# Performance work log

Measured on AMD Instinct MI355X. Metric: run time of the kernel, lower is better.

## Reference

```python
import jax, jax.numpy as jnp
import numpy as np

B, LQ, LIM = 4, 640, 1296
D_MODEL, NHEAD, DFF, MAX_DIST = 768, 12, 3072, 100
DK = D_MODEL // NHEAD
EPS = 1e-5


def _layer_norm(x, g, b):
    mu = jnp.mean(x, axis=-1, keepdims=True)
    var = jnp.mean(jnp.square(x - mu), axis=-1, keepdims=True)
    return (x - mu) * jax.lax.rsqrt(var + EPS) * g + b


def setup_inputs() -> dict:
    key = jax.random.key(0)
    ks = jax.random.split(key, 24)
    s = 0.02
    inp = {
        "docqa": jax.random.normal(ks[0], (B, LQ, D_MODEL), jnp.float32),
        "im_tokens": jax.random.normal(ks[1], (B, LIM, D_MODEL), jnp.float32),
        "docqa_x": jax.random.randint(ks[2], (B, LQ), 0, 1000, jnp.int32),
        "docqa_y": jax.random.randint(ks[3], (B, LQ), 0, 1000, jnp.int32),
        "im_tokens_x": jax.random.randint(ks[4], (B, LIM), 0, 1000, jnp.int32),
        "im_tokens_y": jax.random.randint(ks[5], (B, LIM), 0, 1000, jnp.int32),
        # attention projection params
        "Wq": jax.random.normal(ks[6], (D_MODEL, D_MODEL), jnp.float32) * s,
        "bq": jnp.zeros((D_MODEL,), jnp.float32),
        "Wk": jax.random.normal(ks[7], (D_MODEL, D_MODEL), jnp.float32) * s,
        "bk": jnp.zeros((D_MODEL,), jnp.float32),
        "Wv": jax.random.normal(ks[8], (D_MODEL, D_MODEL), jnp.float32) * s,
        "bv": jnp.zeros((D_MODEL,), jnp.float32),
        "Wo": jax.random.normal(ks[9], (D_MODEL, D_MODEL), jnp.float32) * s,
        "bo": jnp.zeros((D_MODEL,), jnp.float32),
        # relative position bias tables: (2*max_dist+1, nhead) per axis
        "bias_x": jax.random.normal(ks[10], (2 * MAX_DIST + 1, NHEAD), jnp.float32) * s,
        "bias_y": jax.random.normal(ks[11], (2 * MAX_DIST + 1, NHEAD), jnp.float32) * s,
        # FFN
        "W1": jax.random.normal(ks[12], (D_MODEL, DFF), jnp.float32) * s,
        "b1": jnp.zeros((DFF,), jnp.float32),
        "W2": jax.random.normal(ks[13], (DFF, D_MODEL), jnp.float32) * s,
        "b2": jnp.zeros((D_MODEL,), jnp.float32),
        # LayerNorms
        "g1": jnp.ones((D_MODEL,), jnp.float32),
        "be1": jnp.zeros((D_MODEL,), jnp.float32),
        "g2": jnp.ones((D_MODEL,), jnp.float32),
        "be2": jnp.zeros((D_MODEL,), jnp.float32),
    }
    return inp


def reference(docqa, im_tokens, docqa_x, docqa_y, im_tokens_x, im_tokens_y,
              Wq, bq, Wk, bk, Wv, bv, Wo, bo, bias_x, bias_y,
              W1, b1, W2, b2, g1, be1, g2, be2):
    # keys/values attend over concatenated image tokens + docqa tokens
    full = jnp.concatenate([im_tokens, docqa], axis=1)            # (B, Lk, D)
    full_x = jnp.concatenate([im_tokens_x, docqa_x], axis=1)      # (B, Lk)
    full_y = jnp.concatenate([im_tokens_y, docqa_y], axis=1)

    q = (docqa @ Wq + bq).reshape(B, LQ, NHEAD, DK)               # (B,Lq,H,Dk)
    k = (full @ Wk + bk).reshape(B, LQ + LIM, NHEAD, DK)
    v = (full @ Wv + bv).reshape(B, LQ + LIM, NHEAD, DK)

    scores = jnp.einsum("bqhd,bkhd->bhqk", q, k) / jnp.sqrt(jnp.float32(DK))

    # relative-position bias, clamped to [-max_dist, max_dist]
    rel_x = jnp.clip(docqa_x[:, :, None] - full_x[:, None, :], -MAX_DIST, MAX_DIST) + MAX_DIST
    rel_y = jnp.clip(docqa_y[:, :, None] - full_y[:, None, :], -MAX_DIST, MAX_DIST) + MAX_DIST
    pos_bias = bias_x[rel_x] + bias_y[rel_y]                      # (B,Lq,Lk,H)
    scores = scores + jnp.transpose(pos_bias, (0, 3, 1, 2))       # (B,H,Lq,Lk)

    attn = jax.nn.softmax(scores, axis=-1)
    ctx = jnp.einsum("bhqk,bkhd->bqhd", attn, v).reshape(B, LQ, D_MODEL)
    attn_out = ctx @ Wo + bo

    # residual + norm + FFN + residual + norm (dropout=0 in eval)
    src = _layer_norm(docqa + attn_out, g1, be1)
    ffn = jnp.maximum(src @ W1 + b1, 0.0) @ W2 + b2
    src = _layer_norm(src + ffn, g2, be2)
    return src
```

## Files before the change

kernel.cpp:

```cpp
#include <hip/hip_runtime.h>
#include <hip/hip_bf16.h>

constexpr int B      = 4;
constexpr int LQ     = 640;
constexpr int LIM    = 1296;
constexpr int LK     = LQ + LIM;
constexpr int DM     = 768;
constexpr int NHEAD  = 12;
constexpr int DK     = 64;
constexpr int DFF    = 3072;
constexpr int MAXD   = 100;
constexpr int M_DOC  = B * LQ;
constexpr int M_FULL = B * LK;
constexpr size_t ML_CNT = (size_t)B * NHEAD * LQ;

typedef __attribute__((ext_vector_type(8))) short bf16x8_t;
typedef __attribute__((ext_vector_type(4))) float f32x4_t;

__device__ __forceinline__ float b2f(__hip_bfloat16 x) { return __bfloat162float(x); }

__device__ __forceinline__ float ldf(const void* p, size_t i, int f32flag) {
    return f32flag ? ((const float*)p)[i]
                   : b2f(((const __hip_bfloat16*)p)[i]);
}

__device__ __forceinline__ void gl_lds16(const void* g, void* l) {
    __builtin_amdgcn_global_load_lds(
        (const __attribute__((address_space(1))) unsigned int*)g,
        (__attribute__((address_space(3))) unsigned int*)l, 16, 0, 0);
}

__global__ __launch_bounds__(256)
void prep_kernel(const void* __restrict__ g1, int* __restrict__ flagp,
                 const int* __restrict__ dqx, const int* __restrict__ dqy,
                 const int* __restrict__ imx, const int* __restrict__ imy,
                 int* __restrict__ cx, int* __restrict__ cy)
{
    if (blockIdx.x == 0 && threadIdx.x == 0) {
        unsigned u = *(const unsigned*)g1;
        *flagp = ((u & 0xFFFFu) == 0u) ? 1 : 0;
    }
    int idx = blockIdx.x * 256 + threadIdx.x;
    for (; idx < B * LK; idx += gridDim.x * 256) {
        int b = idx / LK, l = idx - b * LK;
        cx[idx] = (l < LIM) ? imx[b * LIM + l] : dqx[b * LQ + l - LIM];
        cy[idx] = (l < LIM) ? imy[b * LIM + l] : dqy[b * LQ + l - LIM];
    }
}

__device__ __forceinline__ void wtrans_tile(const void* W, __hip_bfloat16* Wt,
                                            int f32, int K, int N, int n0, int k0,
                                            __hip_bfloat16 (*t)[33])
{
    const int tx = threadIdx.x & 31, ty = threadIdx.x >> 5;
#pragma unroll
    for (int j = 0; j < 4; ++j) {
        int k = ty + j * 8;
        t[k][tx] = __float2bfloat16(ldf(W, (size_t)(k0 + k) * N + n0 + tx, f32));
    }
    __syncthreads();
#pragma unroll
    for (int j = 0; j < 4; ++j) {
        int n = ty + j * 8;
        Wt[(size_t)(n0 + n) * K + k0 + tx] = t[tx][n];
    }
}

__global__ __launch_bounds__(256)
void wtransA_kernel(const void* __restrict__ Wq, const void* __restrict__ Wk,
                    const void* __restrict__ Wv, const void* __restrict__ Wo,
                    __hip_bfloat16* __restrict__ Wt3, __hip_bfloat16* __restrict__ WtO,
                    const int* __restrict__ flagp)
{
    __shared__ __hip_bfloat16 t[32][33];
    const int f32 = *flagp;
    const int bx  = blockIdx.x;
    const int wid = bx / 576;
    const int tt  = bx % 576;
    const void* W = (wid == 0) ? Wq : (wid == 1) ? Wk : (wid == 2) ? Wv : Wo;
    __hip_bfloat16* dst = (wid == 3) ? WtO : Wt3 + (size_t)wid * DM * DM;
    wtrans_tile(W, dst, f32, DM, DM, (tt % 24) * 32, (tt / 24) * 32, t);
}

__global__ __launch_bounds__(256)
void wtransW_kernel(const void* __restrict__ W1, const void* __restrict__ W2,
                    __hip_bfloat16* __restrict__ W1t, __hip_bfloat16* __restrict__ W2t,
                    const int* __restrict__ flagp)
{
    __shared__ __hip_bfloat16 t[32][33];
    const int f32 = *flagp;
    int bx = blockIdx.x;
    const bool second = bx >= 2304;
    const void* W = second ? W2 : W1;
    __hip_bfloat16* dst = second ? W2t : W1t;
    const int K = second ? DFF : DM;
    const int N = second ? DM : DFF;
    const int tt = second ? bx - 2304 : bx;
    const int nt = N / 32;
    wtrans_tile(W, dst, f32, K, N, (tt % nt) * 32, (tt / nt) * 32, t);
}

__global__ __launch_bounds__(256)
void qkv_gemm(const void* __restrict__ Aim,
              const void* __restrict__ Adoc,
              const __hip_bfloat16* __restrict__ Wt3,
              const void* __restrict__ bq,
              const void* __restrict__ bk,
              const void* __restrict__ bv,
              __hip_bfloat16* __restrict__ qb,
              __hip_bfloat16* __restrict__ kb,
              __hip_bfloat16* __restrict__ vtb,
              const int* __restrict__ flagp)
{
    __shared__ __hip_bfloat16 Als[128 * 32];
    __shared__ __hip_bfloat16 Bls[128 * 32];

    const int f32  = *flagp;
    const int tid  = threadIdx.x;
    const int lane = tid & 63;
    const int wave = tid >> 6;
    const int quad = lane >> 4;
    const int c16  = lane & 15;
    const int n0   = blockIdx.x * 128;
    const int m0   = blockIdx.y * 128;
    const int wm   = (wave >> 1) * 64;
    const int wn   = (wave & 1) * 64;
    constexpr int K = DM;

    f32x4_t acc[4][4] = {};

    for (int k0 = 0; k0 < K; k0 += 32) {
#pragma unroll
        for (int p = 0; p < 2; ++p) {
            const int lin = p * 64 + lane;
            int row = wave * 32 + (lin >> 2);
            int gr  = m0 + row; if (gr > M_FULL - 1) gr = M_FULL - 1;
            const int kcol = k0 + (lin & 3) * 8;
            int bb = gr / LK;
            int l  = gr - bb * LK;
            const void* base; size_t roff;
            if (l < LIM) { base = Aim;  roff = (size_t)(bb * LIM + l) * K; }
            else         { base = Adoc; roff = (size_t)(bb * LQ + (l - LIM)) * K; }
            union { bf16x8_t v; __hip_bfloat16 h[8]; } pk;
            if (f32) {
                const float4* fp = (const float4*)((const float*)base + roff + kcol);
                float4 a = fp[0], b4 = fp[1];
                pk.h[0] = __float2bfloat16(a.x);  pk.h[1] = __float2bfloat16(a.y);
                pk.h[2] = __float2bfloat16(a.z);  pk.h[3] = __float2bfloat16(a.w);
                pk.h[4] = __float2bfloat16(b4.x); pk.h[5] = __float2bfloat16(b4.y);
                pk.h[6] = __float2bfloat16(b4.z); pk.h[7] = __float2bfloat16(b4.w);
            } else {
                pk.v = *(const bf16x8_t*)((const __hip_bfloat16*)base + roff + kcol);
            }
            *(bf16x8_t*)(Als + wave * 1024 + (size_t)lin * 8) = pk.v;
        }
#pragma unroll
        for (int p = 0; p < 2; ++p) {
            const int lin = p * 64 + lane;
            const int row = wave * 32 + (lin >> 2);
            gl_lds16(Wt3 + (size_t)(n0 + row) * K + k0 + (lin & 3) * 8,
                     Bls + wave * 1024 + p * 512);
        }
        __syncthreads();

        bf16x8_t af[4], bfr[4];
#pragma unroll
        for (int i = 0; i < 4; ++i)
            af[i] = *(const bf16x8_t*)(Als + (wm + i * 16 + c16) * 32 + quad * 8);
#pragma unroll
        for (int j = 0; j < 4; ++j)
            bfr[j] = *(const bf16x8_t*)(Bls + (wn + j * 16 + c16) * 32 + quad * 8);
#pragma unroll
        for (int i = 0; i < 4; ++i)
#pragma unroll
            for (int j = 0; j < 4; ++j)
                acc[i][j] = __builtin_amdgcn_mfma_f32_16x16x32_bf16(af[i], bfr[j], acc[i][j], 0, 0, 0);
        __syncthreads();
    }

    const int seg = n0 / DM;
    const void* bptr = (seg == 0) ? bq : (seg == 1) ? bk : bv;
#pragma unroll
    for (int j = 0; j < 4; ++j) {
        const int col  = n0 + wn + j * 16 + c16;
        const int ncol = col - seg * DM;
        const float bj = ldf(bptr, ncol, f32);
        if (seg == 2) {
            const int h = ncol >> 6, d = ncol & 63;
#pragma unroll
            for (int i = 0; i < 4; ++i) {
                const int rowb = m0 + wm + i * 16 + quad * 4;
                const int bb0  = rowb / LK;
                const int l0   = rowb - bb0 * LK;
                if (l0 + 3 < LK && rowb + 3 < M_FULL) {
                    union { ushort4 u4; __hip_bfloat16 hh[4]; } pk;
#pragma unroll
                    for (int r = 0; r < 4; ++r)
                        pk.hh[r] = __float2bfloat16(acc[i][j][r] + bj);
                    *(ushort4*)(vtb + ((size_t)((bb0 * NHEAD + h) * DK + d)) * LK + l0) = pk.u4;
                } else {
#pragma unroll
                    for (int r = 0; r < 4; ++r) {
                        const int row = rowb + r;
                        if (row < M_FULL) {
                            int bb = row / LK, l = row - bb * LK;
                            vtb[((size_t)((bb * NHEAD + h) * DK + d)) * LK + l] =
                                __float2bfloat16(acc[i][j][r] + bj);
                        }
                    }
                }
            }
        } else {
            const float scl = (seg == 0) ? 0.125f : 1.f;
#pragma unroll
            for (int i = 0; i < 4; ++i) {
                const int rowb = m0 + wm + i * 16 + quad * 4;
#pragma unroll
                for (int r = 0; r < 4; ++r) {
                    const int row = rowb + r;
                    if (row < M_FULL) {
                        __hip_bfloat16 hv = __float2bfloat16((acc[i][j][r] + bj) * scl);
                        if (seg == 1) kb[(size_t)row * DM + ncol] = hv;
                        else {
                            int bb = row / LK, l = row - bb * LK;
                            if (l >= LIM)
                                qb[(size_t)(bb * LQ + (l - LIM)) * DM + ncol] = hv;
                        }
                    }
                }
            }
        }
    }
}

__global__ __launch_bounds__(256)
void mfma_gemm_relu(const __hip_bfloat16* __restrict__ Abf,
                    const __hip_bfloat16* __restrict__ Wt,
                    const void* __restrict__ bias,
                    __hip_bfloat16* __restrict__ Cc,
                    const int* __restrict__ flagp,
                    int M, int N, int K)
{
    __shared__ __hip_bfloat16 Als[128 * 32];
    __shared__ __hip_bfloat16 Bls[128 * 32];

    const int f32  = *flagp;
    const int tid  = threadIdx.x;
    const int lane = tid & 63;
    const int wave = tid >> 6;
    const int quad = lane >> 4;
    const int c16  = lane & 15;
    const int n0   = blockIdx.x * 128;
    const int m0   = blockIdx.y * 128;
    const int wm   = (wave >> 1) * 64;
    const int wn   = (wave & 1) * 64;

    f32x4_t acc[4][4] = {};

    for (int k0 = 0; k0 < K; k0 += 32) {
#pragma unroll
        for (int p = 0; p < 2; ++p) {
            const int lin = p * 64 + lane;
            int row = wave * 32 + (lin >> 2);
            int gr  = m0 + row; if (gr > M - 1) gr = M - 1;
            gl_lds16(Abf + (size_t)gr * K + k0 + (lin & 3) * 8, Als + wave * 1024 + p * 512);
        }
#pragma unroll
        for (int p = 0; p < 2; ++p) {
            const int lin = p * 64 + lane;
            const int row = wave * 32 + (lin >> 2);
            gl_lds16(Wt + (size_t)(n0 + row) * K + k0 + (lin & 3) * 8,
                     Bls + wave * 1024 + p * 512);
        }
        __syncthreads();

        bf16x8_t af[4], bfr[4];
#pragma unroll
        for (int i = 0; i < 4; ++i)
            af[i] = *(const bf16x8_t*)(Als + (wm + i * 16 + c16) * 32 + quad * 8);
#pragma unroll
        for (int j = 0; j < 4; ++j)
            bfr[j] = *(const bf16x8_t*)(Bls + (wn + j * 16 + c16) * 32 + quad * 8);
#pragma unroll
        for (int i = 0; i < 4; ++i)
#pragma unroll
            for (int j = 0; j < 4; ++j)
                acc[i][j] = __builtin_amdgcn_mfma_f32_16x16x32_bf16(af[i], bfr[j], acc[i][j], 0, 0, 0);
        __syncthreads();
    }

#pragma unroll
    for (int j = 0; j < 4; ++j) {
        const int col = n0 + wn + j * 16 + c16;
        const float bj = ldf(bias, col, f32);
#pragma unroll
        for (int i = 0; i < 4; ++i) {
            const int rowb = m0 + wm + i * 16 + quad * 4;
#pragma unroll
            for (int r = 0; r < 4; ++r) {
                const int row = rowb + r;
                if (row < M) {
                    float v = fmaxf(acc[i][j][r] + bj, 0.f);
                    Cc[(size_t)row * N + col] = __float2bfloat16(v);
                }
            }
        }
    }
}

__global__ __launch_bounds__(256)
void sk_gemm(const __hip_bfloat16* __restrict__ Abf,
             const __hip_bfloat16* __restrict__ Wt,
             float* __restrict__ Cc,
             int M, int N, int K, int S)
{
    __shared__ __hip_bfloat16 Als[128 * 32];
    __shared__ __hip_bfloat16 Bls[128 * 32];

    const int tid  = threadIdx.x;
    const int lane = tid & 63;
    const int wave = tid >> 6;
    const int quad = lane >> 4;
    const int c16  = lane & 15;
    const int n0   = blockIdx.x * 128;
    const int m0   = blockIdx.y * 128;
    const int wm   = (wave >> 1) * 64;
    const int wn   = (wave & 1) * 64;
    const int kchunk = K / S;
    const int kbeg = blockIdx.z * kchunk;

    f32x4_t acc[4][4] = {};

    for (int k0 = kbeg; k0 < kbeg + kchunk; k0 += 32) {
#pragma unroll
        for (int p = 0; p < 2; ++p) {
            const int lin = p * 64 + lane;
            int row = wave * 32 + (lin >> 2);
            int gr  = m0 + row; if (gr > M - 1) gr = M - 1;
            gl_lds16(Abf + (size_t)gr * K + k0 + (lin & 3) * 8, Als + wave * 1024 + p * 512);
        }
#pragma unroll
        for (int p = 0; p < 2; ++p) {
            const int lin = p * 64 + lane;
            const int row = wave * 32 + (lin >> 2);
            gl_lds16(Wt + (size_t)(n0 + row) * K + k0 + (lin & 3) * 8,
                     Bls + wave * 1024 + p * 512);
        }
        __syncthreads();

        bf16x8_t af[4], bfr[4];
#pragma unroll
        for (int i = 0; i < 4; ++i)
            af[i] = *(const bf16x8_t*)(Als + (wm + i * 16 + c16) * 32 + quad * 8);
#pragma unroll
        for (int j = 0; j < 4; ++j)
            bfr[j] = *(const bf16x8_t*)(Bls + (wn + j * 16 + c16) * 32 + quad * 8);
#pragma unroll
        for (int i = 0; i < 4; ++i)
#pragma unroll
            for (int j = 0; j < 4; ++j)
                acc[i][j] = __builtin_amdgcn_mfma_f32_16x16x32_bf16(af[i], bfr[j], acc[i][j], 0, 0, 0);
        __syncthreads();
    }

#pragma unroll
    for (int j = 0; j < 4; ++j) {
        const int col = n0 + wn + j * 16 + c16;
#pragma unroll
        for (int i = 0; i < 4; ++i) {
            const int rowb = m0 + wm + i * 16 + quad * 4;
#pragma unroll
            for (int r = 0; r < 4; ++r) {
                const int row = rowb + r;
                if (row < M) atomicAdd(&Cc[(size_t)row * N + col], acc[i][j][r]);
            }
        }
    }
}

__global__ __launch_bounds__(256)
void attn_part_kernel(const __hip_bfloat16* __restrict__ Qb,
                      const __hip_bfloat16* __restrict__ Kb,
                      const __hip_bfloat16* __restrict__ Vtb,
                      const int* __restrict__ cx, const int* __restrict__ cy,
                      const void* __restrict__ bias_x,
                      const void* __restrict__ bias_y,
                      __hip_bfloat16* __restrict__ p0,
                      __hip_bfloat16* __restrict__ p1,
                      float* __restrict__ mlbase,
                      const int* __restrict__ flagp)
{
    constexpr int QT = 64, KT = 64;
    constexpr int QROW = 72;
    __shared__ __hip_bfloat16 Ps[QT * QROW];
    __shared__ float bxs[2 * MAXD + 1], bys[2 * MAXD + 1];

    const int f32  = *flagp;
    const int tid  = threadIdx.x;
    const int lane = tid & 63;
    const int wave = tid >> 6;
    const int quad = lane >> 4;
    const int c16  = lane & 15;
    const int h    = blockIdx.y;
    const int b    = blockIdx.z & 3;
    const int s    = blockIdx.z >> 2;
    const int q0   = blockIdx.x * QT;
    const int kbeg = s * 1024;
    const int kend = s ? LK : 1024;

    __hip_bfloat16* Op = s ? p1 : p0;
    float* mp = mlbase + (size_t)s * 2 * ML_CNT;
    float* lp = mp + ML_CNT;

    for (int i = tid; i < 2 * MAXD + 1; i += 256) {
        bxs[i] = ldf(bias_x, (size_t)i * NHEAD + h, f32);
        bys[i] = ldf(bias_y, (size_t)i * NHEAD + h, f32);
    }

    const __hip_bfloat16* qrow = Qb + ((size_t)(b * LQ + q0 + wave * 16 + c16)) * DM + h * DK;
    const bf16x8_t aq0 = *(const bf16x8_t*)(qrow + quad * 8);
    const bf16x8_t aq1 = *(const bf16x8_t*)(qrow + 32 + quad * 8);
    int qx[4], qy[4];
#pragma unroll
    for (int r = 0; r < 4; ++r) {
        const int qi = b * LK + LIM + q0 + wave * 16 + quad * 4 + r;
        qx[r] = cx[qi]; qy[r] = cy[qi];
    }
    const __hip_bfloat16* vrow = Vtb + ((size_t)((b * NHEAD + h) * DK)) * LK;

    __syncthreads();

    f32x4_t O[4] = {};
    float m_r[4], l_r[4];
#pragma unroll
    for (int r = 0; r < 4; ++r) { m_r[r] = -1e30f; l_r[r] = 0.f; }

    for (int k0 = kbeg; k0 < kend; k0 += KT) {
        f32x4_t S[4];
#pragma unroll
        for (int jn = 0; jn < 4; ++jn) {
            int krow = k0 + jn * 16 + c16; if (krow > LK - 1) krow = LK - 1;
            const __hip_bfloat16* kr = Kb + ((size_t)(b * LK + krow)) * DM + h * DK;
            bf16x8_t bk0 = *(const bf16x8_t*)(kr + quad * 8);
            bf16x8_t bk1 = *(const bf16x8_t*)(kr + 32 + quad * 8);
            f32x4_t acc = {0.f, 0.f, 0.f, 0.f};
            acc = __builtin_amdgcn_mfma_f32_16x16x32_bf16(aq0, bk0, acc, 0, 0, 0);
            acc = __builtin_amdgcn_mfma_f32_16x16x32_bf16(aq1, bk1, acc, 0, 0, 0);
            S[jn] = acc;
        }
#pragma unroll
        for (int jn = 0; jn < 4; ++jn) {
            const int kg = k0 + jn * 16 + c16;
            const bool ok = kg < LK;
            const int kgc = ok ? kg : LK - 1;
            const int kx = cx[b * LK + kgc], ky = cy[b * LK + kgc];
#pragma unroll
            for (int r = 0; r < 4; ++r) {
                int rx = min(max(qx[r] - kx, -MAXD), MAXD) + MAXD;
                int ry = min(max(qy[r] - ky, -MAXD), MAXD) + MAXD;
                float v = S[jn][r] + bxs[rx] + bys[ry];
                S[jn][r] = ok ? v : -1e30f;
            }
        }
        float alpha[4];
#pragma unroll
        for (int r = 0; r < 4; ++r) {
            float mx = fmaxf(fmaxf(S[0][r], S[1][r]), fmaxf(S[2][r], S[3][r]));
            mx = fmaxf(mx, __shfl_xor(mx, 1));
            mx = fmaxf(mx, __shfl_xor(mx, 2));
            mx = fmaxf(mx, __shfl_xor(mx, 4));
            mx = fmaxf(mx, __shfl_xor(mx, 8));
            const float mt = fmaxf(m_r[r], mx);
            const float al = __expf(m_r[r] - mt);
            float sum = 0.f;
#pragma unroll
            for (int jn = 0; jn < 4; ++jn) {
                float p = __expf(S[jn][r] - mt);
                S[jn][r] = p;
                sum += p;
            }
            sum += __shfl_xor(sum, 1);
            sum += __shfl_xor(sum, 2);
            sum += __shfl_xor(sum, 4);
            sum += __shfl_xor(sum, 8);
            m_r[r] = mt;
            l_r[r] = l_r[r] * al + sum;
            alpha[r] = al;
        }
#pragma unroll
        for (int jn = 0; jn < 4; ++jn)
#pragma unroll
            for (int r = 0; r < 4; ++r)
                Ps[(wave * 16 + quad * 4 + r) * QROW + jn * 16 + c16] = __float2bfloat16(S[jn][r]);
#pragma unroll
        for (int jd = 0; jd < 4; ++jd)
#pragma unroll
            for (int r = 0; r < 4; ++r) O[jd][r] *= alpha[r];
        bf16x8_t ap0 = *(const bf16x8_t*)(Ps + (wave * 16 + c16) * QROW + quad * 8);
        bf16x8_t ap1 = *(const bf16x8_t*)(Ps + (wave * 16 + c16) * QROW + 32 + quad * 8);
        int kc0 = k0 + quad * 8;      if (kc0 > LK - 8) kc0 = LK - 8;
        int kc1 = k0 + 32 + quad * 8; if (kc1 > LK - 8) kc1 = LK - 8;
#pragma unroll
        for (int jd = 0; jd < 4; ++jd) {
            const __hip_bfloat16* vr = vrow + (size_t)(jd * 16 + c16) * LK;
            bf16x8_t bv0 = *(const bf16x8_t*)(vr + kc0);
            bf16x8_t bv1 = *(const bf16x8_t*)(vr + kc1);
            O[jd] = __builtin_amdgcn_mfma_f32_16x16x32_bf16(ap0, bv0, O[jd], 0, 0, 0);
            O[jd] = __builtin_amdgcn_mfma_f32_16x16x32_bf16(ap1, bv1, O[jd], 0, 0, 0);
        }
    }

#pragma unroll
    for (int r = 0; r < 4; ++r) {
        const int ql = wave * 16 + quad * 4 + r;
        const size_t grow = (size_t)(b * LQ + q0 + ql);
#pragma unroll
        for (int jd = 0; jd < 4; ++jd)
            Op[grow * DM + h * DK + jd * 16 + c16] = __float2bfloat16(O[jd][r]);
        if (c16 == 0) {
            size_t mli = ((size_t)b * NHEAD + h) * LQ + q0 + ql;
            mp[mli] = m_r[r];
            lp[mli] = l_r[r];
        }
    }
}

__global__ __launch_bounds__(256)
void attn_merge_kernel(const __hip_bfloat16* __restrict__ p0,
                       const __hip_bfloat16* __restrict__ p1,
                       const float* __restrict__ mlbase,
                       __hip_bfloat16* __restrict__ ctx,
                       float* __restrict__ aof)
{
    const int row = blockIdx.x;
    const int b = row / LQ, q = row - b * LQ;
    const int tid = threadIdx.x;
#pragma unroll
    for (int i = 0; i < 3; ++i) {
        const int c = tid + i * 256;
        const int h = c >> 6;
        const size_t mli = ((size_t)b * NHEAD + h) * LQ + q;
        const float m0 = mlbase[mli],              l0 = mlbase[ML_CNT + mli];
        const float m1 = mlbase[2 * ML_CNT + mli], l1 = mlbase[3 * ML_CNT + mli];
        const float mm = fmaxf(m0, m1);
        const float w0 = __expf(m0 - mm), w1 = __expf(m1 - mm);
        const float denom = l0 * w0 + l1 * w1;
        const size_t idx = (size_t)row * DM + c;
        const float v = (b2f(p0[idx]) * w0 + b2f(p1[idx]) * w1) / denom;
        ctx[idx] = __float2bfloat16(v);
        aof[idx] = 0.f;
    }
}

template<int MODE>
__global__ __launch_bounds__(256)
void ln_kernel(const void* __restrict__ Xin,
               const __hip_bfloat16* __restrict__ Xb,
               const float* __restrict__ Xf2f,
               const void* __restrict__ bias2,
               const void* __restrict__ g,
               const void* __restrict__ be,
               __hip_bfloat16* __restrict__ outb,
               void* __restrict__ outv,
               float* __restrict__ zbuf,
               const int* __restrict__ flagp)
{
    __shared__ float red1[256], red2[256];
    const int f32 = *flagp;
    const int row = blockIdx.x;
    const int tid = threadIdx.x;

    float x[3];
#pragma unroll
    for (int i = 0; i < 3; ++i) {
        int c = tid + i * 256;
        size_t idx = (size_t)row * DM + c;
        float a  = (MODE == 0) ? ldf(Xin, idx, f32) : b2f(Xb[idx]);
        x[i] = a + Xf2f[idx] + ldf(bias2, c, f32);
    }
    float s1 = x[0] + x[1] + x[2];
    float s2 = x[0] * x[0] + x[1] * x[1] + x[2] * x[2];
    red1[tid] = s1;
    red2[tid] = s2;
    __syncthreads();
    for (int off = 128; off > 0; off >>= 1) {
        if (tid < off) {
            red1[tid] += red1[tid + off];
            red2[tid] += red2[tid + off];
        }
        __syncthreads();
    }
    float mu   = red1[0] * (1.f / DM);
    float var  = red2[0] * (1.f / DM) - mu * mu;
    float rstd = rsqrtf(var + 1e-5f);
#pragma unroll
    for (int i = 0; i < 3; ++i) {
        int c = tid + i * 256;
        size_t idx = (size_t)row * DM + c;
        float v = (x[i] - mu) * rstd * ldf(g, c, f32) + ldf(be, c, f32);
        if (MODE == 0) {
            outb[idx] = __float2bfloat16(v);
            zbuf[idx] = 0.f;
        } else {
            if (f32) ((float*)outv)[idx] = v;
            else     ((__hip_bfloat16*)outv)[idx] = __float2bfloat16(v);
        }
    }
}

extern "C" void kernel_launch(void* const* d_in, const int* in_sizes, int n_in,
                              void* d_out, int out_size, void* d_ws, size_t ws_size,
                              hipStream_t stream)
{
    const void* docqa = d_in[0];
    const void* im    = d_in[1];
    const int* dqx = (const int*)d_in[2];
    const int* dqy = (const int*)d_in[3];
    const int* imx = (const int*)d_in[4];
    const int* imy = (const int*)d_in[5];
    const void* Wq = d_in[6];
    const void* bq = d_in[7];
    const void* Wk = d_in[8];
    const void* bk = d_in[9];
    const void* Wv = d_in[10];
    const void* bv = d_in[11];
    const void* Wo = d_in[12];
    const void* bo = d_in[13];
    const void* bias_x = d_in[14];
    const void* bias_y = d_in[15];
    const void* W1 = d_in[16];
    const void* b1 = d_in[17];
    const void* W2 = d_in[18];
    const void* b2 = d_in[19];
    const void* g1  = d_in[20];
    const void* be1 = d_in[21];
    const void* g2  = d_in[22];
    const void* be2 = d_in[23];

    char* w = (char*)d_ws;
    int*            flagp = (int*)w;
    __hip_bfloat16* qb  = (__hip_bfloat16*)(w + 256);
    __hip_bfloat16* kb  = qb + (size_t)M_DOC  * DM;
    __hip_bfloat16* vtb = kb + (size_t)M_FULL * DM;
    __hip_bfloat16* cb  = vtb + (size_t)M_FULL * DM;
    char* cbB = (char*)cb;

    __hip_bfloat16* Wt3  = cb;
    __hip_bfloat16* p0   = cb;
    __hip_bfloat16* p1   = (__hip_bfloat16*)(cbB + 3932160);
    float*          mlb  = (float*)(cbB + 7864320);
    __hip_bfloat16* WtO  = (__hip_bfloat16*)(cbB + 8355840);
    int*            cxp  = (int*)(cbB + 9535488);
    int*            cyp  = cxp + (size_t)B * LK;
    __hip_bfloat16* ctx  = cb;
    __hip_bfloat16* src1 = cb;
    float*          fof  = (float*)(cbB + 3932160);
    float*          aof  = (float*)vtb;
    __hip_bfloat16* W1t  = vtb;
    __hip_bfloat16* W2t  = vtb + (size_t)DFF * DM;
    __hip_bfloat16* mid  = qb;

    dim3 blk(256);

    prep_kernel<<<dim3(32), blk, 0, stream>>>(g1, flagp, dqx, dqy, imx, imy, cxp, cyp);
    wtransA_kernel<<<dim3(4 * 576), blk, 0, stream>>>(Wq, Wk, Wv, Wo, Wt3, WtO, flagp);
    qkv_gemm<<<dim3(3 * DM / 128, (M_FULL + 127) / 128), blk, 0, stream>>>(
        im, docqa, Wt3, bq, bk, bv, qb, kb, vtb, flagp);
    attn_part_kernel<<<dim3(LQ / 64, NHEAD, B * 2), blk, 0, stream>>>(
        qb, kb, vtb, cxp, cyp, bias_x, bias_y, p0, p1, mlb, flagp);
    attn_merge_kernel<<<dim3(M_DOC), blk, 0, stream>>>(p0, p1, mlb, ctx, aof);
    sk_gemm<<<dim3(DM / 128, M_DOC / 128, 4), blk, 0, stream>>>(
        ctx, WtO, aof, M_DOC, DM, DM, 4);
    ln_kernel<0><<<dim3(M_DOC), blk, 0, stream>>>(
        docqa, nullptr, aof, bo, g1, be1, src1, nullptr, fof, flagp);
    wtransW_kernel<<<dim3(2 * 2304), blk, 0, stream>>>(W1, W2, W1t, W2t, flagp);
    mfma_gemm_relu<<<dim3(DFF / 128, M_DOC / 128), blk, 0, stream>>>(
        src1, W1t, b1, mid, flagp, M_DOC, DFF, DM);
    sk_gemm<<<dim3(DM / 128, M_DOC / 128, 4), blk, 0, stream>>>(
        mid, W2t, fof, M_DOC, DM, DFF, 4);
    ln_kernel<1><<<dim3(M_DOC), blk, 0, stream>>>(
        nullptr, src1, fof, b2, g2, be2, nullptr, d_out, nullptr, flagp);
}
```

Measured before the change: 451.2 us.

## Pre-convert concatenated input to bf16 and load QKV GEMM A via LDS DMA

```diff
diff --git a/kernel.cpp b/kernel.cpp
--- a/kernel.cpp
+++ b/kernel.cpp
@@ -31,21 +31,34 @@
 }
 
 __global__ __launch_bounds__(256)
-void prep_kernel(const void* __restrict__ g1, int* __restrict__ flagp,
-                 const int* __restrict__ dqx, const int* __restrict__ dqy,
-                 const int* __restrict__ imx, const int* __restrict__ imy,
-                 int* __restrict__ cx, int* __restrict__ cy)
-{
-    if (blockIdx.x == 0 && threadIdx.x == 0) {
-        unsigned u = *(const unsigned*)g1;
-        *flagp = ((u & 0xFFFFu) == 0u) ? 1 : 0;
-    }
-    int idx = blockIdx.x * 256 + threadIdx.x;
-    for (; idx < B * LK; idx += gridDim.x * 256) {
-        int b = idx / LK, l = idx - b * LK;
-        cx[idx] = (l < LIM) ? imx[b * LIM + l] : dqx[b * LQ + l - LIM];
-        cy[idx] = (l < LIM) ? imy[b * LIM + l] : dqy[b * LQ + l - LIM];
-    }
+void prep_conv_kernel(const void* __restrict__ g1, int* __restrict__ flagp,
+                      const void* __restrict__ im, const void* __restrict__ docqa,
+                      __hip_bfloat16* __restrict__ fullA)
+{
+    const bool f32 = ((*(const unsigned*)g1) & 0xFFFFu) == 0u;
+    if (blockIdx.x == 0 && threadIdx.x == 0) *flagp = f32 ? 1 : 0;
+
+    const int chunk = blockIdx.x * 256 + threadIdx.x;
+    if (chunk >= M_FULL * (DM / 8)) return;
+    const int row = chunk / (DM / 8);
+    const int col = (chunk - row * (DM / 8)) * 8;
+    const int b   = row / LK;
+    const int l   = row - b * LK;
+    const size_t srow = (l < LIM) ? ((size_t)(b * LIM + l)) * DM
+                                  : ((size_t)(b * LQ + (l - LIM))) * DM;
+    const void* src = (l < LIM) ? im : docqa;
+    union { bf16x8_t v; __hip_bfloat16 h[8]; } pk;
+    if (f32) {
+        const float4* fp = (const float4*)((const float*)src + srow + col);
+        float4 a = fp[0], c = fp[1];
+        pk.h[0] = __float2bfloat16(a.x); pk.h[1] = __float2bfloat16(a.y);
+        pk.h[2] = __float2bfloat16(a.z); pk.h[3] = __float2bfloat16(a.w);
+        pk.h[4] = __float2bfloat16(c.x); pk.h[5] = __float2bfloat16(c.y);
+        pk.h[6] = __float2bfloat16(c.z); pk.h[7] = __float2bfloat16(c.w);
+    } else {
+        pk.v = *(const bf16x8_t*)((const __hip_bfloat16*)src + srow + col);
+    }
+    *(bf16x8_t*)(fullA + (size_t)row * DM + col) = pk.v;
 }
 
 __device__ __forceinline__ void wtrans_tile(const void* W, __hip_bfloat16* Wt,
@@ -67,19 +80,27 @@
 }
 
 __global__ __launch_bounds__(256)
-void wtransA_kernel(const void* __restrict__ Wq, const void* __restrict__ Wk,
-                    const void* __restrict__ Wv, const void* __restrict__ Wo,
-                    __hip_bfloat16* __restrict__ Wt3, __hip_bfloat16* __restrict__ WtO,
+void wtrans3_kernel(const void* __restrict__ Wq, const void* __restrict__ Wk,
+                    const void* __restrict__ Wv, __hip_bfloat16* __restrict__ Wt3,
                     const int* __restrict__ flagp)
 {
     __shared__ __hip_bfloat16 t[32][33];
     const int f32 = *flagp;
-    const int bx  = blockIdx.x;
-    const int wid = bx / 576;
-    const int tt  = bx % 576;
-    const void* W = (wid == 0) ? Wq : (wid == 1) ? Wk : (wid == 2) ? Wv : Wo;
-    __hip_bfloat16* dst = (wid == 3) ? WtO : Wt3 + (size_t)wid * DM * DM;
-    wtrans_tile(W, dst, f32, DM, DM, (tt % 24) * 32, (tt / 24) * 32, t);
+    const int wid = blockIdx.x / 576;
+    const int tt  = blockIdx.x % 576;
+    const void* W = (wid == 0) ? Wq : (wid == 1) ? Wk : Wv;
+    wtrans_tile(W, Wt3 + (size_t)wid * DM * DM, f32, DM, DM,
+                (tt % 24) * 32, (tt / 24) * 32, t);
+}
+
+__global__ __launch_bounds__(256)
+void wtransO_kernel(const void* __restrict__ Wo, __hip_bfloat16* __restrict__ WtO,
+                    const int* __restrict__ flagp)
+{
+    __shared__ __hip_bfloat16 t[32][33];
+    const int f32 = *flagp;
+    const int tt  = blockIdx.x;
+    wtrans_tile(Wo, WtO, f32, DM, DM, (tt % 24) * 32, (tt / 24) * 32, t);
 }
 
 __global__ __launch_bounds__(256)
@@ -101,13 +122,12 @@
 }
 
 __global__ __launch_bounds__(256)
-void qkv_gemm(const void* __restrict__ Aim,
-              const void* __restrict__ Adoc,
+void qkv_gemm(const __hip_bfloat16* __restrict__ fullA,
               const __hip_bfloat16* __restrict__ Wt3,
               const void* __restrict__ bq,
               const void* __restrict__ bk,
               const void* __restrict__ bv,
-              __hip_bfloat16* __restrict__ qb,
+              __hip_bfloat16* __restrict__ qout,
               __hip_bfloat16* __restrict__ kb,
               __hip_bfloat16* __restrict__ vtb,
               const int* __restrict__ flagp)
@@ -135,24 +155,8 @@
             const int lin = p * 64 + lane;
             int row = wave * 32 + (lin >> 2);
             int gr  = m0 + row; if (gr > M_FULL - 1) gr = M_FULL - 1;
-            const int kcol = k0 + (lin & 3) * 8;
-            int bb = gr / LK;
-            int l  = gr - bb * LK;
-            const void* base; size_t roff;
-            if (l < LIM) { base = Aim;  roff = (size_t)(bb * LIM + l) * K; }
-            else         { base = Adoc; roff = (size_t)(bb * LQ + (l - LIM)) * K; }
-            union { bf16x8_t v; __hip_bfloat16 h[8]; } pk;
-            if (f32) {
-                const float4* fp = (const float4*)((const float*)base + roff + kcol);
-                float4 a = fp[0], b4 = fp[1];
-                pk.h[0] = __float2bfloat16(a.x);  pk.h[1] = __float2bfloat16(a.y);
-                pk.h[2] = __float2bfloat16(a.z);  pk.h[3] = __float2bfloat16(a.w);
-                pk.h[4] = __float2bfloat16(b4.x); pk.h[5] = __float2bfloat16(b4.y);
-                pk.h[6] = __float2bfloat16(b4.z); pk.h[7] = __float2bfloat16(b4.w);
-            } else {
-                pk.v = *(const bf16x8_t*)((const __hip_bfloat16*)base + roff + kcol);
-            }
-            *(bf16x8_t*)(Als + wave * 1024 + (size_t)lin * 8) = pk.v;
+            gl_lds16(fullA + (size_t)gr * K + k0 + (lin & 3) * 8,
+                     Als + wave * 1024 + p * 512);
         }
 #pragma unroll
         for (int p = 0; p < 2; ++p) {
@@ -224,7 +228,7 @@
                         else {
                             int bb = row / LK, l = row - bb * LK;
                             if (l >= LIM)
-                                qb[(size_t)(bb * LQ + (l - LIM)) * DM + ncol] = hv;
+                                qout[(size_t)(bb * LQ + (l - LIM)) * DM + ncol] = hv;
                         }
                     }
                 }
@@ -382,7 +386,8 @@
 void attn_part_kernel(const __hip_bfloat16* __restrict__ Qb,
                       const __hip_bfloat16* __restrict__ Kb,
                       const __hip_bfloat16* __restrict__ Vtb,
-                      const int* __restrict__ cx, const int* __restrict__ cy,
+                      const int* __restrict__ dqx, const int* __restrict__ dqy,
+                      const int* __restrict__ imx, const int* __restrict__ imy,
                       const void* __restrict__ bias_x,
                       const void* __restrict__ bias_y,
                       __hip_bfloat16* __restrict__ p0,
@@ -423,8 +428,8 @@
     int qx[4], qy[4];
 #pragma unroll
     for (int r = 0; r < 4; ++r) {
-        const int qi = b * LK + LIM + q0 + wave * 16 + quad * 4 + r;
-        qx[r] = cx[qi]; qy[r] = cy[qi];
+        const int qi = b * LQ + q0 + wave * 16 + quad * 4 + r;
+        qx[r] = dqx[qi]; qy[r] = dqy[qi];
     }
     const __hip_bfloat16* vrow = Vtb + ((size_t)((b * NHEAD + h) * DK)) * LK;
 
@@ -453,7 +458,8 @@
             const int kg = k0 + jn * 16 + c16;
             const bool ok = kg < LK;
             const int kgc = ok ? kg : LK - 1;
-            const int kx = cx[b * LK + kgc], ky = cy[b * LK + kgc];
+            const int kx = (kgc < LIM) ? imx[b * LIM + kgc] : dqx[b * LQ + kgc - LIM];
+            const int ky = (kgc < LIM) ? imy[b * LIM + kgc] : dqy[b * LQ + kgc - LIM];
 #pragma unroll
             for (int r = 0; r < 4; ++r) {
                 int rx = min(max(qx[r] - kx, -MAXD), MAXD) + MAXD;
@@ -639,36 +645,38 @@
 
     char* w = (char*)d_ws;
     int*            flagp = (int*)w;
-    __hip_bfloat16* qb  = (__hip_bfloat16*)(w + 256);
-    __hip_bfloat16* kb  = qb + (size_t)M_DOC  * DM;
+    __hip_bfloat16* qR  = (__hip_bfloat16*)(w + 256);
+    __hip_bfloat16* kb  = qR + (size_t)M_DOC  * DM;
     __hip_bfloat16* vtb = kb + (size_t)M_FULL * DM;
     __hip_bfloat16* cb  = vtb + (size_t)M_FULL * DM;
     char* cbB = (char*)cb;
 
-    __hip_bfloat16* Wt3  = cb;
+    __hip_bfloat16* fullA = cb;
+    __hip_bfloat16* Wt3  = qR;
+    __hip_bfloat16* WtO  = qR;
+    __hip_bfloat16* qout = (__hip_bfloat16*)d_out;
     __hip_bfloat16* p0   = cb;
     __hip_bfloat16* p1   = (__hip_bfloat16*)(cbB + 3932160);
     float*          mlb  = (float*)(cbB + 7864320);
-    __hip_bfloat16* WtO  = (__hip_bfloat16*)(cbB + 8355840);
-    int*            cxp  = (int*)(cbB + 9535488);
-    int*            cyp  = cxp + (size_t)B * LK;
     __hip_bfloat16* ctx  = cb;
     __hip_bfloat16* src1 = cb;
     float*          fof  = (float*)(cbB + 3932160);
     float*          aof  = (float*)vtb;
     __hip_bfloat16* W1t  = vtb;
     __hip_bfloat16* W2t  = vtb + (size_t)DFF * DM;
-    __hip_bfloat16* mid  = qb;
+    __hip_bfloat16* mid  = qR;
 
     dim3 blk(256);
 
-    prep_kernel<<<dim3(32), blk, 0, stream>>>(g1, flagp, dqx, dqy, imx, imy, cxp, cyp);
-    wtransA_kernel<<<dim3(4 * 576), blk, 0, stream>>>(Wq, Wk, Wv, Wo, Wt3, WtO, flagp);
+    prep_conv_kernel<<<dim3((M_FULL * (DM / 8) + 255) / 256), blk, 0, stream>>>(
+        g1, flagp, im, docqa, fullA);
+    wtrans3_kernel<<<dim3(3 * 576), blk, 0, stream>>>(Wq, Wk, Wv, Wt3, flagp);
     qkv_gemm<<<dim3(3 * DM / 128, (M_FULL + 127) / 128), blk, 0, stream>>>(
-        im, docqa, Wt3, bq, bk, bv, qb, kb, vtb, flagp);
+        fullA, Wt3, bq, bk, bv, qout, kb, vtb, flagp);
     attn_part_kernel<<<dim3(LQ / 64, NHEAD, B * 2), blk, 0, stream>>>(
-        qb, kb, vtb, cxp, cyp, bias_x, bias_y, p0, p1, mlb, flagp);
+        qout, kb, vtb, dqx, dqy, imx, imy, bias_x, bias_y, p0, p1, mlb, flagp);
     attn_merge_kernel<<<dim3(M_DOC), blk, 0, stream>>>(p0, p1, mlb, ctx, aof);
+    wtransO_kernel<<<dim3(576), blk, 0, stream>>>(Wo, WtO, flagp);
     sk_gemm<<<dim3(DM / 128, M_DOC / 128, 4), blk, 0, stream>>>(
         ctx, WtO, aof, M_DOC, DM, DM, 4);
     ln_kernel<0><<<dim3(M_DOC), blk, 0, stream>>>(
```

Result: slower. 483.9 us (+7.2%).
